# Optimization experiments

Hardware: AMD Instinct MI355X
Metric: run time of the kernel (lower is better)

## Reference

```python
import jax, jax.numpy as jnp
import numpy as np

EPS = 1e-5
DIM_HEAD = 64
HEADS = 8

def layernorm(x, gamma, beta):
    mu = jnp.mean(x, axis=-1, keepdims=True)
    var = jnp.var(x, axis=-1, keepdims=True)
    return (x - mu) * jax.lax.rsqrt(var + EPS) * gamma + beta

def setup_inputs() -> dict:
    key = jax.random.key(0)
    ks = jax.random.split(key, 8)
    b, n, dh = 1, 896, 3072       # batch, enformer seq len, enformer_hidden_dim
    c, j, dc = 64, 127, 1024      # num contexts (tracks), context len, context_dim
    inner = HEADS * DIM_HEAD      # 512
    return {
        "embeddings": jax.random.normal(ks[0], (b, n, dh), jnp.float32),
        "context": jax.random.normal(ks[1], (c, j, dc), jnp.float32),
        "context_mask": jax.random.randint(ks[2], (b, j), 0, 2) > 0,
        "q_gamma": jnp.ones((dh,), jnp.float32),
        "q_beta": jnp.zeros((dh,), jnp.float32),
        "kv_gamma": jnp.ones((dc,), jnp.float32),
        "kv_beta": jnp.zeros((dc,), jnp.float32),
        "Wq": jax.random.normal(ks[3], (dh, inner), jnp.float32) * 0.02,
        "Wkv": jax.random.normal(ks[4], (dc, 2 * inner), jnp.float32) * 0.02,
        "null_k": jax.random.normal(ks[5], (inner,), jnp.float32),
        "null_v": jax.random.normal(ks[6], (inner,), jnp.float32),
        "Wo": jax.random.normal(ks[7], (inner, dh), jnp.float32) * 0.02,
        "bo": jnp.zeros((dh,), jnp.float32),
        "Wp": jax.random.normal(jax.random.fold_in(key, 9), (dh, 1), jnp.float32) * 0.02,
        "bp": jnp.zeros((1,), jnp.float32),
    }

def reference(embeddings, context, context_mask, q_gamma, q_beta, kv_gamma, kv_beta,
              Wq, Wkv, null_k, null_v, Wo, bo, Wp, bp):
    h, d = HEADS, DIM_HEAD
    scale = d ** -0.5
    b, n, dh = embeddings.shape
    c = context.shape[0]
    # projections
    q = layernorm(embeddings, q_gamma, q_beta) @ Wq            # (b, n, h*d)
    kv = layernorm(context, kv_gamma, kv_beta) @ Wkv           # (c, j, 2*h*d)
    k, v = jnp.split(kv, 2, axis=-1)
    # prepend null key/value token
    k = jnp.concatenate([jnp.broadcast_to(null_k, (c, 1, h * d)), k], axis=1)
    v = jnp.concatenate([jnp.broadcast_to(null_v, (c, 1, h * d)), v], axis=1)
    # split heads: (b, h, i, d) / (c, h, j, d)
    q = q.reshape(b, n, h, d).transpose(0, 2, 1, 3)
    k = k.reshape(c, -1, h, d).transpose(0, 2, 1, 3)
    v = v.reshape(c, -1, h, d).transpose(0, 2, 1, 3)
    sim = jnp.einsum('bhid,chjd->bchij', q, k) * scale         # (b, c, h, i, j+1)
    # mask: pad with True for the null token, broadcast over c, h, i
    mask = jnp.pad(context_mask, ((0, 0), (1, 0)), constant_values=True)
    sim = jnp.where(mask[:, None, None, None, :], sim, -jnp.finfo(sim.dtype).max)
    attn = jax.nn.softmax(sim, axis=-1)
    out = jnp.einsum('bchij,chjd->bchid', attn, v)             # (b, c, h, i, d)
    out = out.transpose(0, 1, 3, 2, 4).reshape(b, c, n, h * d)  # (b, c, n, h*d)
    branch = out @ Wo + bo                                     # (b, c, n, dh)
    emb = embeddings[:, None] + branch                         # (b, c, n, dh)
    pred = jax.nn.softplus((emb @ Wp + bp)[..., 0])            # (b, c, n)
    return pred.transpose(0, 2, 1)                             # (b, n, c)
```

## Files before the change

### kernel.cpp

```cpp
#include <hip/hip_runtime.h>
#include <math.h>

#define N_SEQ   896
#define DH      3072
#define NCTX    64
#define JLEN    127
#define DC      1024
#define HEADS   8
#define DHEAD   64
#define INNER   512
#define MKV     8128
#define MKVPAD  8192

typedef __bf16 bf16x8 __attribute__((ext_vector_type(8)));
typedef float  f32x4  __attribute__((ext_vector_type(4)));

#define OFF_EDOT   0LL
#define OFF_QBF    (OFF_EDOT + N_SEQ)
#define OFF_KBF    (OFF_QBF  + (long long)N_SEQ*INNER/2)
#define OFF_VPM    (OFF_KBF  + (long long)NCTX*128*INNER/2)
#define OFF_VPNULL (OFF_VPM  + (long long)MKV*8)
#define OFF_WOP    (OFF_VPNULL + 8)
#define OFF_BOP    (OFF_WOP  + INNER)
#define OFF_SBUF   (OFF_BOP  + 16)
#define OFF_ANQ    (OFF_SBUF + (long long)NCTX*HEADS*N_SEQ)
#define OFF_ANKV   (OFF_ANQ  + (long long)N_SEQ*DH/2)
#define OFF_WQT    (OFF_ANKV + (long long)MKVPAD*DC/2)
#define OFF_WKT    (OFF_WQT  + (long long)INNER*DH/2)
#define OFF_WVPT   (OFF_WKT  + (long long)INNER*DC/2)
#define OFF_QSL    (OFF_WVPT + 16*1024/2)

__device__ __forceinline__ void async_copy16(const __bf16* g, __bf16* l) {
    __builtin_amdgcn_global_load_lds(
        (const __attribute__((address_space(1))) unsigned int*)g,
        (__attribute__((address_space(3))) unsigned int*)l,
        16, 0, 0);
}

#define GRIDW  2058

__global__ __launch_bounds__(256)
void prep_w_kernel(const float* __restrict__ Wq, const float* __restrict__ Wkv,
                   const float* __restrict__ Wo, const float* __restrict__ bo,
                   const float* __restrict__ Wp,
                   const float* __restrict__ nullk, const float* __restrict__ nullv,
                   __bf16* __restrict__ WQT, __bf16* __restrict__ WKT,
                   __bf16* __restrict__ WVPT, float* __restrict__ VPNULL,
                   float* __restrict__ BOP, __bf16* __restrict__ KBF)
{
    __shared__ float tT[32][33];
    const int bid = blockIdx.x, tid = threadIdx.x;
    const int lane = tid & 63, wid = tid >> 6;

    if (bid < 8) {
        int h = bid;
        float* wops = &tT[0][0];
        int d = tid >> 2, part = tid & 3;
        const float* worow = Wo + (long long)(h * 64 + d) * DH;
        float s = 0.f;
        #pragma unroll 8
        for (int k = part * 4; k < DH; k += 16) {
            float4 a = *(const float4*)&worow[k];
            float4 w = *(const float4*)&Wp[k];
            s += a.x*w.x + a.y*w.y + a.z*w.z + a.w*w.w;
        }
        s += __shfl_xor(s, 1); s += __shfl_xor(s, 2);
        if (part == 0) wops[d] = s;
        __syncthreads();
        if (tid < 64) {
            float v = nullv[h * 64 + tid] * wops[tid];
            #pragma unroll
            for (int o = 1; o < 64; o <<= 1) v += __shfl_xor(v, o);
            if (tid == 0) VPNULL[h] = v;
        }
        #pragma unroll
        for (int kk = 0; kk < 4; ++kk) {
            int k = tid + kk * 256;
            const float* src = Wkv + (long long)k * (2 * INNER) + INNER + h * 64;
            float s2 = 0.f;
            #pragma unroll
            for (int d2 = 0; d2 < 64; d2 += 4) {
                float4 a = *(const float4*)&src[d2];
                s2 += a.x*wops[d2] + a.y*wops[d2+1] + a.z*wops[d2+2] + a.w*wops[d2+3];
            }
            WVPT[h * 1024 + k] = (__bf16)s2;
        }
    } else if (bid == 8) {
        float* red = &tT[0][0];
        float s = 0.f;
        #pragma unroll
        for (int i = 0; i < 3; ++i) {
            int k = i * 1024 + tid * 4;
            float4 a = *(const float4*)&bo[k];
            float4 w = *(const float4*)&Wp[k];
            s += a.x*w.x + a.y*w.y + a.z*w.z + a.w*w.w;
        }
        #pragma unroll
        for (int o = 1; o < 64; o <<= 1) s += __shfl_xor(s, o);
        if (lane == 0) red[wid] = s;
        __syncthreads();
        if (tid == 0) *BOP = red[0] + red[1] + red[2] + red[3];
    } else if (bid == 9) {
        for (int i = tid; i < 8 * 1024; i += 256)
            WVPT[8 * 1024 + i] = (__bf16)0.f;
        for (int i = tid; i < NCTX * INNER; i += 256) {
            int c = i >> 9, d2 = i & 511;
            KBF[(long long)(c * 128) * INNER + d2] = (__bf16)nullk[d2];
        }
    } else {
        int t = bid - 10;
        const float* src; __bf16* dst; int srcS, dstS, rb, cb;
        if (t < 1536) {
            rb = (t >> 4) * 32; cb = (t & 15) * 32;
            src = Wq; srcS = INNER; dst = WQT; dstS = DH;
        } else {
            int bi = t - 1536;
            rb = (bi >> 4) * 32; cb = (bi & 15) * 32;
            src = Wkv; srcS = 2 * INNER; dst = WKT; dstS = DC;
        }
        int tx = tid & 31, ty = tid >> 5;
        #pragma unroll
        for (int i = 0; i < 32; i += 8)
            tT[ty + i][tx] = src[(long long)(rb + ty + i) * srcS + cb + tx];
        __syncthreads();
        #pragma unroll
        for (int i = 0; i < 32; i += 8)
            dst[(long long)(cb + ty + i) * dstS + rb + tx] = (__bf16)tT[tx][ty + i];
    }
}

#define B_QL   2032
#define GRIDL  (B_QL + 224)

__global__ __launch_bounds__(256)
void prep_ln_kernel(const float* __restrict__ emb, const float* __restrict__ ctx,
                    const float* __restrict__ qg, const float* __restrict__ qb_,
                    const float* __restrict__ kvg, const float* __restrict__ kvb,
                    const float* __restrict__ Wp,
                    __bf16* __restrict__ ANQ, __bf16* __restrict__ ANKV,
                    float* __restrict__ EDOT)
{
    const int bid = blockIdx.x, tid = threadIdx.x;
    const int lane = tid & 63, wid = tid >> 6;

    if (bid < B_QL) {
        int r = bid * 4 + wid;
        const float* x = ctx + (long long)r * DC;
        f32x4 xv[4];
        float s = 0.f, ss = 0.f;
        #pragma unroll
        for (int c = 0; c < 4; ++c) {
            const f32x4* p = (const f32x4*)&x[c * 256 + lane * 4];
            xv[c] = __builtin_nontemporal_load(p);
            s  += xv[c][0] + xv[c][1] + xv[c][2] + xv[c][3];
            ss += xv[c][0]*xv[c][0] + xv[c][1]*xv[c][1]
                + xv[c][2]*xv[c][2] + xv[c][3]*xv[c][3];
        }
        #pragma unroll
        for (int o = 1; o < 64; o <<= 1) { s += __shfl_xor(s, o); ss += __shfl_xor(ss, o); }
        float m  = s * (1.f / DC);
        float rs = rsqrtf(ss * (1.f / DC) - m * m + 1e-5f);
        __bf16* op = ANKV + (long long)r * DC;
        #pragma unroll
        for (int c = 0; c < 4; ++c) {
            int col = c * 256 + lane * 4;
            float4 g4 = *(const float4*)&kvg[col];
            float4 b4 = *(const float4*)&kvb[col];
            __bf16 ov[4];
            ov[0] = (__bf16)((xv[c][0] - m) * rs * g4.x + b4.x);
            ov[1] = (__bf16)((xv[c][1] - m) * rs * g4.y + b4.y);
            ov[2] = (__bf16)((xv[c][2] - m) * rs * g4.z + b4.z);
            ov[3] = (__bf16)((xv[c][3] - m) * rs * g4.w + b4.w);
            *(ushort4*)&op[col] = *(ushort4*)ov;
        }
    } else {
        int r = (bid - B_QL) * 4 + wid;
        const float* x = emb + (long long)r * DH;
        float s = 0.f, ss = 0.f, dp = 0.f;
        #pragma unroll
        for (int c = 0; c < 12; ++c) {
            int col = c * 256 + lane * 4;
            float4 a = *(const float4*)&x[col];
            float4 w = *(const float4*)&Wp[col];
            s  += a.x + a.y + a.z + a.w;
            ss += a.x*a.x + a.y*a.y + a.z*a.z + a.w*a.w;
            dp += a.x*w.x + a.y*w.y + a.z*w.z + a.w*w.w;
        }
        #pragma unroll
        for (int o = 1; o < 64; o <<= 1) {
            s += __shfl_xor(s, o); ss += __shfl_xor(ss, o); dp += __shfl_xor(dp, o);
        }
        float m  = s * (1.f / DH);
        float rs = rsqrtf(ss * (1.f / DH) - m * m + 1e-5f);
        __bf16* op = ANQ + (long long)r * DH;
        #pragma unroll
        for (int c = 0; c < 12; ++c) {
            int col = c * 256 + lane * 4;
            float4 a  = *(const float4*)&x[col];
            float4 g4 = *(const float4*)&qg[col];
            float4 b4 = *(const float4*)&qb_[col];
            __bf16 ov[4];
            ov[0] = (__bf16)((a.x - m) * rs * g4.x + b4.x);
            ov[1] = (__bf16)((a.y - m) * rs * g4.y + b4.y);
            ov[2] = (__bf16)((a.z - m) * rs * g4.z + b4.z);
            ov[3] = (__bf16)((a.w - m) * rs * g4.w + b4.w);
            *(ushort4*)&op[col] = *(ushort4*)ov;
        }
        if (lane == 0) EDOT[r] = dp;
    }
}

__global__ __launch_bounds__(256)
void proj_kernel(const __bf16* __restrict__ ANQ, const __bf16* __restrict__ WQT,
                 const __bf16* __restrict__ ANKV, const __bf16* __restrict__ WKT,
                 const __bf16* __restrict__ WVPT,
                 float* __restrict__ qsl, __bf16* __restrict__ kout,
                 float* __restrict__ vpm) {
    __shared__ __align__(16) __bf16 As[128 * 32];
    __shared__ __align__(16) __bf16 Bs[128 * 32];
    int b = blockIdx.x;
    int tid = threadIdx.x;
    int lane = tid & 63, w = tid >> 6;
    int n16 = lane & 15, quad = lane >> 4;
    int wr = (w >> 1) * 64, wc = (w & 1) * 64;

    const __bf16 *A, *B;
    int K, kbeg, kend, mode, slice = 0;
    long long m0, n0;
    if (b < 224) {
        mode = 0; slice = b / 28;
        int rem = b % 28;
        m0 = (long long)(rem % 7) * 128;
        n0 = (long long)(rem / 7) * 128;
        K = DH; kbeg = slice * 384; kend = kbeg + 384;
        A = ANQ; B = WQT;
    } else {
        mode = 1;
        int b2 = b - 224;
        m0 = (long long)(b2 & 63) * 128;
        n0 = (long long)(b2 >> 6) * 128;
        K = DC; kbeg = 0; kend = DC;
        A = ANKV; B = WKT;
    }
    bool dovp = (mode == 1) && (n0 == 0);

    const __bf16* aG = A + (m0 + (tid >> 2)) * K + (tid & 3) * 8;
    const __bf16* bG = B + (n0 + (tid >> 2)) * K + (tid & 3) * 8;
    __bf16* aL = As + tid * 8;
    __bf16* bL = Bs + tid * 8;

    f32x4 acc[4][4], accv[4];
    const f32x4 z = {0.f, 0.f, 0.f, 0.f};
    #pragma unroll
    for (int i = 0; i < 4; ++i) {
        accv[i] = z;
        #pragma unroll
        for (int j = 0; j < 4; ++j) acc[i][j] = z;
    }

    for (int k0 = kbeg; k0 < kend; k0 += 32) {
        async_copy16(aG + k0, aL);
        async_copy16(aG + (long long)64 * K + k0, aL + 2048);
        async_copy16(bG + k0, bL);
        async_copy16(bG + (long long)64 * K + k0, bL + 2048);
        bf16x8 bv;
        if (dovp) bv = *(const bf16x8*)&WVPT[n16 * 1024 + k0 + quad * 8];
        __syncthreads();
        bf16x8 af[4], bfr[4];
        #pragma unroll
        for (int i = 0; i < 4; ++i)
            af[i]  = *(const bf16x8*)&As[(wr + i * 16 + n16) * 32 + quad * 8];
        #pragma unroll
        for (int j = 0; j < 4; ++j)
            bfr[j] = *(const bf16x8*)&Bs[(wc + j * 16 + n16) * 32 + quad * 8];
        #pragma unroll
        for (int i = 0; i < 4; ++i)
            #pragma unroll
            for (int j = 0; j < 4; ++j)
                acc[i][j] = __builtin_amdgcn_mfma_f32_16x16x32_bf16(af[i], bfr[j], acc[i][j], 0, 0, 0);
        if (dovp) {
            #pragma unroll
            for (int i = 0; i < 4; ++i)
                accv[i] = __builtin_amdgcn_mfma_f32_16x16x32_bf16(af[i], bv, accv[i], 0, 0, 0);
        }
        __syncthreads();
    }

    if (mode == 0) {
        float* qdst = qsl + (long long)slice * (N_SEQ * INNER);
        #pragma unroll
        for (int i = 0; i < 4; ++i)
            #pragma unroll
            for (int r = 0; r < 4; ++r) {
                long long gr = m0 + wr + i * 16 + quad * 4 + r;
                #pragma unroll
                for (int j = 0; j < 4; ++j) {
                    long long gc = n0 + wc + j * 16 + n16;
                    qdst[gr * INNER + gc] = acc[i][j][r];
                }
            }
    } else {
        #pragma unroll
        for (int i = 0; i < 4; ++i)
            #pragma unroll
            for (int r = 0; r < 4; ++r) {
                long long gr = m0 + wr + i * 16 + quad * 4 + r;
                if (gr >= MKV) continue;
                int cc = (int)(gr / JLEN), jj = (int)(gr % JLEN);
                #pragma unroll
                for (int j = 0; j < 4; ++j) {
                    long long gc = n0 + wc + j * 16 + n16;
                    kout[((long long)(cc * 128) + jj + 1) * INNER + gc] = (__bf16)acc[i][j][r];
                }
                if (dovp && n16 < 8) vpm[gr * 8 + n16] = accv[i][r];
            }
    }
}

__global__ __launch_bounds__(256)
void qreduce_kernel(const float* __restrict__ qsl, __bf16* __restrict__ qbf) {
    int i = blockIdx.x * 256 + threadIdx.x;
    float4 s4 = {0.f, 0.f, 0.f, 0.f};
    #pragma unroll
    for (int k = 0; k < 8; ++k) {
        float4 a = *(const float4*)&qsl[(long long)k * (N_SEQ * INNER) + i * 4];
        s4.x += a.x; s4.y += a.y; s4.z += a.z; s4.w += a.w;
    }
    __bf16 ov[4] = {(__bf16)s4.x, (__bf16)s4.y, (__bf16)s4.z, (__bf16)s4.w};
    *(ushort4*)&qbf[i * 4] = *(ushort4*)ov;
}

#define KROW 72

__global__ __launch_bounds__(256)
void attn_mfma_kernel(const __bf16* __restrict__ qb, const __bf16* __restrict__ kb,
                      const float* __restrict__ vpm, const float* __restrict__ vpnull,
                      const int* __restrict__ mask, float* __restrict__ s_buf) {
    __shared__ __align__(16) __bf16 ksh[128 * KROW];
    __shared__ float vpsh[128];
    __shared__ float amsh[128];
    int ch = blockIdx.x;
    int h = ch & 7, c = ch >> 3;
    int tid = threadIdx.x;
    int lane = tid & 63, w = tid >> 6;
    int n16 = lane & 15, quad = lane >> 4;

    const __bf16* kbase = kb + (long long)(c * 128) * INNER + h * DHEAD;
    #pragma unroll
    for (int p = 0; p < 4; ++p) {
        int chunk = tid + p * 256;
        int row = chunk >> 3, o = chunk & 7;
        bf16x8 v = *(const bf16x8*)(kbase + (long long)row * INNER + o * 8);
        *(bf16x8*)&ksh[row * KROW + o * 8] = v;
    }
    if (tid < 128) {
        vpsh[tid] = (tid == 0) ? vpnull[h] : vpm[(long long)(c * JLEN + tid - 1) * 8 + h];
        amsh[tid] = (tid == 0) ? 0.f : (mask[tid - 1] ? 0.f : -3.0e38f);
    }
    __syncthreads();

    bf16x8 bF[8][2];
    #pragma unroll
    for (int t = 0; t < 8; ++t)
        #pragma unroll
        for (int s = 0; s < 2; ++s)
            bF[t][s] = *(const bf16x8*)&ksh[(t * 16 + n16) * KROW + s * 32 + quad * 8];

    float vpv[8], am[8];
    #pragma unroll
    for (int t = 0; t < 8; ++t) {
        vpv[t] = vpsh[t * 16 + n16];
        am[t]  = amsh[t * 16 + n16];
    }

    const __bf16* qbase = qb + h * DHEAD;
    const f32x4 zero = {0.f, 0.f, 0.f, 0.f};

    for (int xi = 0; xi < 7; ++xi) {
        bf16x8 aF[2][2];
        int r0s[2];
        #pragma unroll
        for (int it2 = 0; it2 < 2; ++it2) {
            int tile = xi * 8 + it2 * 4 + w;
            r0s[it2] = tile * 16;
            const __bf16* qrow = qbase + (long long)(r0s[it2] + n16) * INNER + quad * 8;
            aF[it2][0] = *(const bf16x8*)(qrow);
            aF[it2][1] = *(const bf16x8*)(qrow + 32);
        }

        #pragma unroll
        for (int it2 = 0; it2 < 2; ++it2) {
            int r0 = r0s[it2];
            f32x4 acc[8];
            #pragma unroll
            for (int t = 0; t < 8; ++t) {
                acc[t] = __builtin_amdgcn_mfma_f32_16x16x32_bf16(aF[it2][0], bF[t][0], zero,   0, 0, 0);
                acc[t] = __builtin_amdgcn_mfma_f32_16x16x32_bf16(aF[it2][1], bF[t][1], acc[t], 0, 0, 0);
            }
            float mloc = -3.0e38f;
            #pragma unroll
            for (int t = 0; t < 8; ++t)
                #pragma unroll
                for (int r = 0; r < 4; ++r)
                    mloc = fmaxf(mloc, acc[t][r] * 0.125f + am[t]);
            #pragma unroll
            for (int o = 1; o < 16; o <<= 1) mloc = fmaxf(mloc, __shfl_xor(mloc, o, 16));
            float lr[4] = {0.f, 0.f, 0.f, 0.f}, pr[4] = {0.f, 0.f, 0.f, 0.f};
            #pragma unroll
            for (int t = 0; t < 8; ++t) {
                #pragma unroll
                for (int r = 0; r < 4; ++r) {
                    float e = __expf(acc[t][r] * 0.125f + am[t] - mloc);
                    lr[r] += e; pr[r] += e * vpv[t];
                }
            }
            #pragma unroll
            for (int o = 1; o < 16; o <<= 1) {
                #pragma unroll
                for (int r = 0; r < 4; ++r) {
                    lr[r] += __shfl_xor(lr[r], o, 16);
                    pr[r] += __shfl_xor(pr[r], o, 16);
                }
            }
            if (n16 == 0) {
                #pragma unroll
                for (int r = 0; r < 4; ++r)
                    s_buf[(long long)ch * N_SEQ + r0 + quad * 4 + r] = pr[r] / lr[r];
            }
        }
    }
}

__global__ void final_kernel(const float* __restrict__ s_buf,
                             const float* __restrict__ e_dot,
                             const float* __restrict__ bop,
                             const float* __restrict__ bp,
                             float* __restrict__ out) {
    int t = blockIdx.x * blockDim.x + threadIdx.x;
    if (t >= N_SEQ * NCTX) return;
    int n = t >> 6, c = t & 63;
    float s = 0.f;
    #pragma unroll
    for (int h = 0; h < HEADS; ++h) s += s_buf[((long long)(c * HEADS + h)) * N_SEQ + n];
    float x = e_dot[n] + s + *bop + *bp;
    out[t] = fmaxf(x, 0.f) + log1pf(__expf(-fabsf(x)));
}

extern "C" void kernel_launch(void* const* d_in, const int* in_sizes, int n_in,
                              void* d_out, int out_size, void* d_ws, size_t ws_size,
                              hipStream_t stream) {
    const float* emb   = (const float*)d_in[0];
    const float* ctx   = (const float*)d_in[1];
    const int*   cmask = (const int*)  d_in[2];
    const float* qg    = (const float*)d_in[3];
    const float* qb_   = (const float*)d_in[4];
    const float* kvg   = (const float*)d_in[5];
    const float* kvb   = (const float*)d_in[6];
    const float* Wq    = (const float*)d_in[7];
    const float* Wkv   = (const float*)d_in[8];
    const float* nullk = (const float*)d_in[9];
    const float* nullv = (const float*)d_in[10];
    const float* Wo    = (const float*)d_in[11];
    const float* bo    = (const float*)d_in[12];
    const float* Wp    = (const float*)d_in[13];
    const float* bp    = (const float*)d_in[14];
    float* out  = (float*)d_out;
    float* ws_f = (float*)d_ws;

    float*  EDOT   = ws_f + OFF_EDOT;
    __bf16* QBF    = (__bf16*)(ws_f + OFF_QBF);
    __bf16* KBF    = (__bf16*)(ws_f + OFF_KBF);
    float*  VPM    = ws_f + OFF_VPM;
    float*  VPNULL = ws_f + OFF_VPNULL;
    float*  BOP    = ws_f + OFF_BOP;
    float*  SBUF   = ws_f + OFF_SBUF;
    __bf16* ANQ    = (__bf16*)(ws_f + OFF_ANQ);
    __bf16* ANKV   = (__bf16*)(ws_f + OFF_ANKV);
    __bf16* WQT    = (__bf16*)(ws_f + OFF_WQT);
    __bf16* WKT    = (__bf16*)(ws_f + OFF_WKT);
    __bf16* WVPT   = (__bf16*)(ws_f + OFF_WVPT);
    float*  QSL    = ws_f + OFF_QSL;

    prep_w_kernel<<<GRIDW, 256, 0, stream>>>(
        Wq, Wkv, Wo, bo, Wp, nullk, nullv, WQT, WKT, WVPT, VPNULL, BOP, KBF);
    prep_ln_kernel<<<GRIDL, 256, 0, stream>>>(
        emb, ctx, qg, qb_, kvg, kvb, Wp, ANQ, ANKV, EDOT);
    proj_kernel<<<480, 256, 0, stream>>>(ANQ, WQT, ANKV, WKT, WVPT, QSL, KBF, VPM);
    qreduce_kernel<<<(N_SEQ * INNER) / 1024, 256, 0, stream>>>(QSL, QBF);
    attn_mfma_kernel<<<NCTX * HEADS, 256, 0, stream>>>(
        QBF, KBF, VPM, VPNULL, cmask, SBUF);
    final_kernel<<<(N_SEQ * NCTX + 255) / 256, 256, 0, stream>>>(SBUF, EDOT, BOP, bp, out);
}
```

Before: 229.7 us.

## Spread Wo·Wp and Wkv·wop folding across many blocks over two prep kernels

The Wo·Wp row reductions, previously done by just 8 blocks (one per head) with a serial dependent Wkv fold, are now spread over 512 blocks, one per Wo row, in the first prep kernel. The results go to a workspace buffer (WOP). The WVPT fold and the VPNULL computation move into the second prep kernel, where they run as 33 extra blocks alongside the layernorm work. This removes the long tail that the 8 heavy blocks created in the weight-prep kernel. The cost is an extra global round-trip through WOP and a cross-kernel dependency.

After: 219.3 us. 1.05x faster.

```diff
diff --git a/kernel.cpp b/kernel.cpp
--- a/kernel.cpp
+++ b/kernel.cpp
@@ -37,55 +37,40 @@
         16, 0, 0);
 }
 
-#define GRIDW  2058
+#define A_BOP  512
+#define A_MISC 513
+#define A_T0   514
+#define GRIDA  (A_T0 + 2048)
 
 __global__ __launch_bounds__(256)
-void prep_w_kernel(const float* __restrict__ Wq, const float* __restrict__ Wkv,
+void prep_a_kernel(const float* __restrict__ Wq, const float* __restrict__ Wkv,
                    const float* __restrict__ Wo, const float* __restrict__ bo,
-                   const float* __restrict__ Wp,
-                   const float* __restrict__ nullk, const float* __restrict__ nullv,
+                   const float* __restrict__ Wp, const float* __restrict__ nullk,
                    __bf16* __restrict__ WQT, __bf16* __restrict__ WKT,
-                   __bf16* __restrict__ WVPT, float* __restrict__ VPNULL,
+                   __bf16* __restrict__ WVPT, float* __restrict__ WOP,
                    float* __restrict__ BOP, __bf16* __restrict__ KBF)
 {
     __shared__ float tT[32][33];
     const int bid = blockIdx.x, tid = threadIdx.x;
     const int lane = tid & 63, wid = tid >> 6;
 
-    if (bid < 8) {
-        int h = bid;
-        float* wops = &tT[0][0];
-        int d = tid >> 2, part = tid & 3;
-        const float* worow = Wo + (long long)(h * 64 + d) * DH;
+    if (bid < 512) {
+        const float* worow = Wo + (long long)bid * DH;
         float s = 0.f;
-        #pragma unroll 8
-        for (int k = part * 4; k < DH; k += 16) {
-            float4 a = *(const float4*)&worow[k];
-            float4 w = *(const float4*)&Wp[k];
+        #pragma unroll
+        for (int c = 0; c < 3; ++c) {
+            int col = c * 1024 + tid * 4;
+            float4 a = *(const float4*)&worow[col];
+            float4 w = *(const float4*)&Wp[col];
             s += a.x*w.x + a.y*w.y + a.z*w.z + a.w*w.w;
         }
-        s += __shfl_xor(s, 1); s += __shfl_xor(s, 2);
-        if (part == 0) wops[d] = s;
-        __syncthreads();
-        if (tid < 64) {
-            float v = nullv[h * 64 + tid] * wops[tid];
-            #pragma unroll
-            for (int o = 1; o < 64; o <<= 1) v += __shfl_xor(v, o);
-            if (tid == 0) VPNULL[h] = v;
-        }
-        #pragma unroll
-        for (int kk = 0; kk < 4; ++kk) {
-            int k = tid + kk * 256;
-            const float* src = Wkv + (long long)k * (2 * INNER) + INNER + h * 64;
-            float s2 = 0.f;
-            #pragma unroll
-            for (int d2 = 0; d2 < 64; d2 += 4) {
-                float4 a = *(const float4*)&src[d2];
-                s2 += a.x*wops[d2] + a.y*wops[d2+1] + a.z*wops[d2+2] + a.w*wops[d2+3];
-            }
-            WVPT[h * 1024 + k] = (__bf16)s2;
-        }
-    } else if (bid == 8) {
+        #pragma unroll
+        for (int o = 1; o < 64; o <<= 1) s += __shfl_xor(s, o);
+        float* red = &tT[0][0];
+        if (lane == 0) red[wid] = s;
+        __syncthreads();
+        if (tid == 0) WOP[bid] = red[0] + red[1] + red[2] + red[3];
+    } else if (bid == A_BOP) {
         float* red = &tT[0][0];
         float s = 0.f;
         #pragma unroll
@@ -100,7 +85,7 @@
         if (lane == 0) red[wid] = s;
         __syncthreads();
         if (tid == 0) *BOP = red[0] + red[1] + red[2] + red[3];
-    } else if (bid == 9) {
+    } else if (bid == A_MISC) {
         for (int i = tid; i < 8 * 1024; i += 256)
             WVPT[8 * 1024 + i] = (__bf16)0.f;
         for (int i = tid; i < NCTX * INNER; i += 256) {
@@ -108,7 +93,7 @@
             KBF[(long long)(c * 128) * INNER + d2] = (__bf16)nullk[d2];
         }
     } else {
-        int t = bid - 10;
+        int t = bid - A_T0;
         const float* src; __bf16* dst; int srcS, dstS, rb, cb;
         if (t < 1536) {
             rb = (t >> 4) * 32; cb = (t & 15) * 32;
@@ -129,22 +114,53 @@
     }
 }
 
-#define B_QL   2032
-#define GRIDL  (B_QL + 224)
+#define B_VPN  32
+#define B_KV0  33
+#define B_Q0   (B_KV0 + 2032)
+#define GRIDB  (B_Q0 + 224)
 
 __global__ __launch_bounds__(256)
-void prep_ln_kernel(const float* __restrict__ emb, const float* __restrict__ ctx,
-                    const float* __restrict__ qg, const float* __restrict__ qb_,
-                    const float* __restrict__ kvg, const float* __restrict__ kvb,
-                    const float* __restrict__ Wp,
-                    __bf16* __restrict__ ANQ, __bf16* __restrict__ ANKV,
-                    float* __restrict__ EDOT)
+void prep_b_kernel(const float* __restrict__ emb, const float* __restrict__ ctx,
+                   const float* __restrict__ qg, const float* __restrict__ qb_,
+                   const float* __restrict__ kvg, const float* __restrict__ kvb,
+                   const float* __restrict__ Wp, const float* __restrict__ Wkv,
+                   const float* __restrict__ nullv, const float* __restrict__ WOP,
+                   __bf16* __restrict__ ANQ, __bf16* __restrict__ ANKV,
+                   __bf16* __restrict__ WVPT, float* __restrict__ VPNULL,
+                   float* __restrict__ EDOT)
 {
+    __shared__ float wsh[512];
     const int bid = blockIdx.x, tid = threadIdx.x;
     const int lane = tid & 63, wid = tid >> 6;
 
-    if (bid < B_QL) {
-        int r = bid * 4 + wid;
+    if (bid < 32) {
+        wsh[tid] = WOP[tid];
+        wsh[tid + 256] = WOP[tid + 256];
+        __syncthreads();
+        int t = bid * 256 + tid;
+        int k = t >> 3, h = t & 7;
+        const float* src = Wkv + (long long)k * (2 * INNER) + INNER + h * 64;
+        const float* wv = &wsh[h * 64];
+        float s = 0.f;
+        #pragma unroll
+        for (int d2 = 0; d2 < 64; d2 += 4) {
+            float4 a = *(const float4*)&src[d2];
+            s += a.x*wv[d2] + a.y*wv[d2+1] + a.z*wv[d2+2] + a.w*wv[d2+3];
+        }
+        WVPT[h * 1024 + k] = (__bf16)s;
+    } else if (bid == B_VPN) {
+        wsh[tid] = WOP[tid];
+        wsh[tid + 256] = WOP[tid + 256];
+        __syncthreads();
+        if (tid < 8) {
+            int h = tid;
+            float s = 0.f;
+            #pragma unroll 16
+            for (int d = 0; d < 64; ++d) s += nullv[h * 64 + d] * wsh[h * 64 + d];
+            VPNULL[h] = s;
+        }
+    } else if (bid < B_Q0) {
+        int r = (bid - B_KV0) * 4 + wid;
         const float* x = ctx + (long long)r * DC;
         f32x4 xv[4];
         float s = 0.f, ss = 0.f;
@@ -174,7 +190,7 @@
             *(ushort4*)&op[col] = *(ushort4*)ov;
         }
     } else {
-        int r = (bid - B_QL) * 4 + wid;
+        int r = (bid - B_Q0) * 4 + wid;
         const float* x = emb + (long long)r * DH;
         float s = 0.f, ss = 0.f, dp = 0.f;
         #pragma unroll
@@ -472,6 +488,7 @@
     __bf16* KBF    = (__bf16*)(ws_f + OFF_KBF);
     float*  VPM    = ws_f + OFF_VPM;
     float*  VPNULL = ws_f + OFF_VPNULL;
+    float*  WOP    = ws_f + OFF_WOP;
     float*  BOP    = ws_f + OFF_BOP;
     float*  SBUF   = ws_f + OFF_SBUF;
     __bf16* ANQ    = (__bf16*)(ws_f + OFF_ANQ);
@@ -481,10 +498,11 @@
     __bf16* WVPT   = (__bf16*)(ws_f + OFF_WVPT);
     float*  QSL    = ws_f + OFF_QSL;
 
-    prep_w_kernel<<<GRIDW, 256, 0, stream>>>(
-        Wq, Wkv, Wo, bo, Wp, nullk, nullv, WQT, WKT, WVPT, VPNULL, BOP, KBF);
-    prep_ln_kernel<<<GRIDL, 256, 0, stream>>>(
-        emb, ctx, qg, qb_, kvg, kvb, Wp, ANQ, ANKV, EDOT);
+    prep_a_kernel<<<GRIDA, 256, 0, stream>>>(
+        Wq, Wkv, Wo, bo, Wp, nullk, WQT, WKT, WVPT, WOP, BOP, KBF);
+    prep_b_kernel<<<GRIDB, 256, 0, stream>>>(
+        emb, ctx, qg, qb_, kvg, kvb, Wp, Wkv, nullv, WOP,
+        ANQ, ANKV, WVPT, VPNULL, EDOT);
     proj_kernel<<<480, 256, 0, stream>>>(ANQ, WQT, ANKV, WKT, WVPT, QSL, KBF, VPM);
     qreduce_kernel<<<(N_SEQ * INNER) / 1024, 256, 0, stream>>>(QSL, QBF);
     attn_mfma_kernel<<<NCTX * HEADS, 256, 0, stream>>>(
```

## Merge weight-prep and layernorm-prep kernels into one launch; restructure Wo·Wp reduction

Applied to the files above, without the earlier changes.

Combines the weight preparation kernel and the layernorm kernel into a single grid with block-index ranges for the heavy Wo·Wp blocks, the KV layernorm, the Q layernorm and the transposes. This removes one launch and lets the independent stages run at the same time. It also changes the per-head Wo·Wp dot product so Wp is staged in shared memory and each wave reduces whole rows with coalesced loads. The cost is a larger shared-memory footprint (about 12 KB) for every block, which may lower occupancy for the light transpose and layernorm blocks.

New measurement: 211.7 us. 7.8% less time.

```diff
diff --git a/kernel.cpp b/kernel.cpp
--- a/kernel.cpp
+++ b/kernel.cpp
@@ -37,35 +37,50 @@
         16, 0, 0);
 }
 
-#define GRIDW  2058
+#define P_KV0  10
+#define P_Q0   (P_KV0 + 2032)
+#define P_T0   (P_Q0 + 224)
+#define GRIDP  (P_T0 + 2048)
 
 __global__ __launch_bounds__(256)
-void prep_w_kernel(const float* __restrict__ Wq, const float* __restrict__ Wkv,
-                   const float* __restrict__ Wo, const float* __restrict__ bo,
-                   const float* __restrict__ Wp,
-                   const float* __restrict__ nullk, const float* __restrict__ nullv,
-                   __bf16* __restrict__ WQT, __bf16* __restrict__ WKT,
-                   __bf16* __restrict__ WVPT, float* __restrict__ VPNULL,
-                   float* __restrict__ BOP, __bf16* __restrict__ KBF)
+void prep_kernel(const float* __restrict__ emb, const float* __restrict__ ctx,
+                 const float* __restrict__ qg, const float* __restrict__ qb_,
+                 const float* __restrict__ kvg, const float* __restrict__ kvb,
+                 const float* __restrict__ Wq, const float* __restrict__ Wkv,
+                 const float* __restrict__ Wo, const float* __restrict__ bo,
+                 const float* __restrict__ Wp,
+                 const float* __restrict__ nullk, const float* __restrict__ nullv,
+                 __bf16* __restrict__ ANQ, __bf16* __restrict__ ANKV,
+                 __bf16* __restrict__ WQT, __bf16* __restrict__ WKT,
+                 __bf16* __restrict__ WVPT, float* __restrict__ VPNULL,
+                 float* __restrict__ EDOT, float* __restrict__ BOP,
+                 __bf16* __restrict__ KBF)
 {
-    __shared__ float tT[32][33];
+    __shared__ __align__(16) float SM[3072 + 64];
     const int bid = blockIdx.x, tid = threadIdx.x;
     const int lane = tid & 63, wid = tid >> 6;
 
     if (bid < 8) {
         int h = bid;
-        float* wops = &tT[0][0];
-        int d = tid >> 2, part = tid & 3;
-        const float* worow = Wo + (long long)(h * 64 + d) * DH;
-        float s = 0.f;
-        #pragma unroll 8
-        for (int k = part * 4; k < DH; k += 16) {
-            float4 a = *(const float4*)&worow[k];
-            float4 w = *(const float4*)&Wp[k];
-            s += a.x*w.x + a.y*w.y + a.z*w.z + a.w*w.w;
-        }
-        s += __shfl_xor(s, 1); s += __shfl_xor(s, 2);
-        if (part == 0) wops[d] = s;
+        float* wpsh = SM;
+        float* wops = SM + 3072;
+        for (int i = tid; i < 768; i += 256)
+            ((f32x4*)wpsh)[i] = ((const f32x4*)Wp)[i];
+        __syncthreads();
+        for (int rr = 0; rr < 16; ++rr) {
+            int d = wid * 16 + rr;
+            const float* worow = Wo + (long long)(h * 64 + d) * DH;
+            float s = 0.f;
+            #pragma unroll
+            for (int c = 0; c < 12; ++c) {
+                int col = c * 256 + lane * 4;
+                float4 a = *(const float4*)&worow[col];
+                s += a.x*wpsh[col] + a.y*wpsh[col+1] + a.z*wpsh[col+2] + a.w*wpsh[col+3];
+            }
+            #pragma unroll
+            for (int o = 1; o < 64; o <<= 1) s += __shfl_xor(s, o);
+            if (lane == 0) wops[d] = s;
+        }
         __syncthreads();
         if (tid < 64) {
             float v = nullv[h * 64 + tid] * wops[tid];
@@ -75,7 +90,7 @@
         }
         #pragma unroll
         for (int kk = 0; kk < 4; ++kk) {
-            int k = tid + kk * 256;
+            int k = kk * 256 + tid;
             const float* src = Wkv + (long long)k * (2 * INNER) + INNER + h * 64;
             float s2 = 0.f;
             #pragma unroll
@@ -86,7 +101,7 @@
             WVPT[h * 1024 + k] = (__bf16)s2;
         }
     } else if (bid == 8) {
-        float* red = &tT[0][0];
+        float* red = SM;
         float s = 0.f;
         #pragma unroll
         for (int i = 0; i < 3; ++i) {
@@ -107,44 +122,8 @@
             int c = i >> 9, d2 = i & 511;
             KBF[(long long)(c * 128) * INNER + d2] = (__bf16)nullk[d2];
         }
-    } else {
-        int t = bid - 10;
-        const float* src; __bf16* dst; int srcS, dstS, rb, cb;
-        if (t < 1536) {
-            rb = (t >> 4) * 32; cb = (t & 15) * 32;
-            src = Wq; srcS = INNER; dst = WQT; dstS = DH;
-        } else {
-            int bi = t - 1536;
-            rb = (bi >> 4) * 32; cb = (bi & 15) * 32;
-            src = Wkv; srcS = 2 * INNER; dst = WKT; dstS = DC;
-        }
-        int tx = tid & 31, ty = tid >> 5;
-        #pragma unroll
-        for (int i = 0; i < 32; i += 8)
-            tT[ty + i][tx] = src[(long long)(rb + ty + i) * srcS + cb + tx];
-        __syncthreads();
-        #pragma unroll
-        for (int i = 0; i < 32; i += 8)
-            dst[(long long)(cb + ty + i) * dstS + rb + tx] = (__bf16)tT[tx][ty + i];
-    }
-}
-
-#define B_QL   2032
-#define GRIDL  (B_QL + 224)
-
-__global__ __launch_bounds__(256)
-void prep_ln_kernel(const float* __restrict__ emb, const float* __restrict__ ctx,
-                    const float* __restrict__ qg, const float* __restrict__ qb_,
-                    const float* __restrict__ kvg, const float* __restrict__ kvb,
-                    const float* __restrict__ Wp,
-                    __bf16* __restrict__ ANQ, __bf16* __restrict__ ANKV,
-                    float* __restrict__ EDOT)
-{
-    const int bid = blockIdx.x, tid = threadIdx.x;
-    const int lane = tid & 63, wid = tid >> 6;
-
-    if (bid < B_QL) {
-        int r = bid * 4 + wid;
+    } else if (bid < P_Q0) {
+        int r = (bid - P_KV0) * 4 + wid;
         const float* x = ctx + (long long)r * DC;
         f32x4 xv[4];
         float s = 0.f, ss = 0.f;
@@ -173,8 +152,8 @@
             ov[3] = (__bf16)((xv[c][3] - m) * rs * g4.w + b4.w);
             *(ushort4*)&op[col] = *(ushort4*)ov;
         }
-    } else {
-        int r = (bid - B_QL) * 4 + wid;
+    } else if (bid < P_T0) {
+        int r = (bid - P_Q0) * 4 + wid;
         const float* x = emb + (long long)r * DH;
         float s = 0.f, ss = 0.f, dp = 0.f;
         #pragma unroll
@@ -207,6 +186,26 @@
             *(ushort4*)&op[col] = *(ushort4*)ov;
         }
         if (lane == 0) EDOT[r] = dp;
+    } else {
+        int t = bid - P_T0;
+        float (*tT)[33] = (float(*)[33])SM;
+        const float* src; __bf16* dst; int srcS, dstS, rb, cb;
+        if (t < 1536) {
+            rb = (t >> 4) * 32; cb = (t & 15) * 32;
+            src = Wq; srcS = INNER; dst = WQT; dstS = DH;
+        } else {
+            int bi = t - 1536;
+            rb = (bi >> 4) * 32; cb = (bi & 15) * 32;
+            src = Wkv; srcS = 2 * INNER; dst = WKT; dstS = DC;
+        }
+        int tx = tid & 31, ty = tid >> 5;
+        #pragma unroll
+        for (int i = 0; i < 32; i += 8)
+            tT[ty + i][tx] = src[(long long)(rb + ty + i) * srcS + cb + tx];
+        __syncthreads();
+        #pragma unroll
+        for (int i = 0; i < 32; i += 8)
+            dst[(long long)(cb + ty + i) * dstS + rb + tx] = (__bf16)tT[tx][ty + i];
     }
 }
 
@@ -481,10 +480,9 @@
     __bf16* WVPT   = (__bf16*)(ws_f + OFF_WVPT);
     float*  QSL    = ws_f + OFF_QSL;
 
-    prep_w_kernel<<<GRIDW, 256, 0, stream>>>(
-        Wq, Wkv, Wo, bo, Wp, nullk, nullv, WQT, WKT, WVPT, VPNULL, BOP, KBF);
-    prep_ln_kernel<<<GRIDL, 256, 0, stream>>>(
-        emb, ctx, qg, qb_, kvg, kvb, Wp, ANQ, ANKV, EDOT);
+    prep_kernel<<<GRIDP, 256, 0, stream>>>(
+        emb, ctx, qg, qb_, kvg, kvb, Wq, Wkv, Wo, bo, Wp, nullk, nullv,
+        ANQ, ANKV, WQT, WKT, WVPT, VPNULL, EDOT, BOP, KBF);
     proj_kernel<<<480, 256, 0, stream>>>(ANQ, WQT, ANKV, WKT, WVPT, QSL, KBF, VPM);
     qreduce_kernel<<<(N_SEQ * INNER) / 1024, 256, 0, stream>>>(QSL, QBF);
     attn_mfma_kernel<<<NCTX * HEADS, 256, 0, stream>>>(
```
